# Performance work log

Hardware: AMD Instinct MI355X
Metric: run time of the kernel (lower is better)

## Reference

```python
import jax, jax.numpy as jnp
import numpy as np

DIM, H, HD = 1024, 16, 64
B, S = 2, 2048
LAMBDA_INIT = 0.8


def _mha(x, wq, bq, wk, bk, wv, bv, wo, bo):
    # x: [B,S,DIM]; wq/wk/wv: [DIM,H,HD]; wo: [H,HD,DIM]
    q = jnp.einsum('btd,dhk->bthk', x, wq) + bq
    k = jnp.einsum('bsd,dhk->bshk', x, wk) + bk
    v = jnp.einsum('bsd,dhk->bshk', x, wv) + bv
    scores = jnp.einsum('bthk,bshk->bhts', q, k) / jnp.sqrt(jnp.asarray(HD, x.dtype))
    attn = jax.nn.softmax(scores, axis=-1)
    out = jnp.einsum('bhts,bshk->bthk', attn, v)
    return jnp.einsum('bthk,hkd->btd', out, wo) + bo


def _get_lambda(lambda_param, layer_idx):
    layer_factor = jnp.clip(jnp.asarray(layer_idx, jnp.float32) * 0.3, 0.0, 5.0)
    offset = 0.6 * jnp.exp(-layer_factor)
    lam = jax.nn.sigmoid(lambda_param) * (1.0 - offset) + 0.2
    return jnp.clip(lam, 0.1, 0.9)


def setup_inputs() -> dict:
    key = jax.random.key(0)
    ks = jax.random.split(key, 10)
    sc_in = 1.0 / np.sqrt(DIM)   # fan-in-ish scale for projections
    sc_out = 1.0 / np.sqrt(H * HD)
    d = {
        'x': jax.random.normal(ks[0], (B, S, DIM), jnp.float32),
        'proj_w': jax.random.normal(ks[1], (DIM, DIM), jnp.float32) * sc_in,
        'proj_b': jnp.zeros((DIM,), jnp.float32),
        'lambda_param': jnp.full((1,), np.log(LAMBDA_INIT) - np.log(1.0 - LAMBDA_INIT), jnp.float32),
        'layer_idx': 0,
    }
    for i, kk in zip((1, 2), (ks[2:6], ks[6:10])):
        d[f'wq{i}'] = jax.random.normal(kk[0], (DIM, H, HD), jnp.float32) * sc_in
        d[f'wk{i}'] = jax.random.normal(kk[1], (DIM, H, HD), jnp.float32) * sc_in
        d[f'wv{i}'] = jax.random.normal(kk[2], (DIM, H, HD), jnp.float32) * sc_in
        d[f'wo{i}'] = jax.random.normal(kk[3], (H, HD, DIM), jnp.float32) * sc_out
        d[f'bq{i}'] = jnp.zeros((H, HD), jnp.float32)
        d[f'bk{i}'] = jnp.zeros((H, HD), jnp.float32)
        d[f'bv{i}'] = jnp.zeros((H, HD), jnp.float32)
        d[f'bo{i}'] = jnp.zeros((DIM,), jnp.float32)
    return d


def reference(x, wq1, bq1, wk1, bk1, wv1, bv1, wo1, bo1,
              wq2, bq2, wk2, bk2, wv2, bv2, wo2, bo2,
              proj_w, proj_b, lambda_param, layer_idx):
    out1 = _mha(x, wq1, bq1, wk1, bk1, wv1, bv1, wo1, bo1)
    out2 = _mha(x, wq2, bq2, wk2, bk2, wv2, bv2, wo2, bo2)
    lam = _get_lambda(lambda_param, layer_idx)  # shape (1,)
    y = (1.0 - lam) * out1 + lam * out2
    return jnp.einsum('btd,de->bte', y, proj_w) + proj_b
```

## Files before the change

### kernel.cpp

```cpp
#include <hip/hip_runtime.h>

#define DEVI __device__ __forceinline__

typedef unsigned short u16;
typedef unsigned int u32;
typedef __bf16 bf16x8 __attribute__((ext_vector_type(8)));
typedef float f32x4 __attribute__((ext_vector_type(4)));
typedef float f32x16 __attribute__((ext_vector_type(16)));
typedef int i32x2v __attribute__((ext_vector_type(2)));

#define SCALE_Q 0.1803368801f

typedef const __attribute__((address_space(1))) void cas1_void;
typedef __attribute__((address_space(3))) void as3_void;

DEVI void lds_dma16(const void* g, void* l) {
  __builtin_amdgcn_global_load_lds((cas1_void*)g, (as3_void*)l, 16, 0, 0);
}

DEVI u16 f2bf(float f) {
  union { float f; u32 u; } v; v.f = f;
  u32 r = v.u + 0x7FFFu + ((v.u >> 16) & 1u);
  return (u16)(r >> 16);
}

DEVI float bf2f(u16 v) {
  union { u32 u; float f; } x; x.u = (u32)v << 16; return x.f;
}

DEVI float exp2n(float x) {
#if __has_builtin(__builtin_amdgcn_exp2f)
  return __builtin_amdgcn_exp2f(x);
#else
  return __expf(x * 0.6931471805599453f);
#endif
}

DEVI u32 pk2(float lo, float hi2) {
  union { __bf16 h[2]; u32 u; } p;
  p.h[0] = (__bf16)lo; p.h[1] = (__bf16)hi2;
  return p.u;
}

DEVI void plswap2(u32 a, u32 b, u32& x, u32& y) {
#if __has_builtin(__builtin_amdgcn_permlane32_swap)
  i32x2v r = __builtin_amdgcn_permlane32_swap((int)a, (int)b, false, false);
  x = (u32)r[0]; y = (u32)r[1];
#else
  u32 ta = __shfl_xor(a, 32), tb = __shfl_xor(b, 32);
  const int hi_ = (int)((threadIdx.x & 63) >> 5);
  x = hi_ ? tb : a;
  y = hi_ ? b : ta;
#endif
}

DEVI float lambda_dev(const float* lamp, const int* lidx) {
  float lf = (float)(*lidx) * 0.3f;
  lf = fminf(fmaxf(lf, 0.0f), 5.0f);
  float offset = 0.6f * expf(-lf);
  float s = 1.0f / (1.0f + expf(-lamp[0]));
  float lam = s * (1.0f - offset) + 0.2f;
  return fminf(fmaxf(lam, 0.1f), 0.9f);
}

__global__ __launch_bounds__(256) void k_cvt(const float* __restrict__ x, u16* __restrict__ o) {
  int i = (blockIdx.x * 256 + threadIdx.x) * 8;
  float4 a = *(const float4*)(x + i);
  float4 b = *(const float4*)(x + i + 4);
  union { u16 s[8]; uint4 v; } r;
  r.s[0] = f2bf(a.x); r.s[1] = f2bf(a.y); r.s[2] = f2bf(a.z); r.s[3] = f2bf(a.w);
  r.s[4] = f2bf(b.x); r.s[5] = f2bf(b.y); r.s[6] = f2bf(b.z); r.s[7] = f2bf(b.w);
  *(uint4*)(o + i) = r.v;
}

struct TransArgs {
  const float* src[9];
  u16* dst[9];
  int smode[9];
  int tmode[9];
};

__global__ __launch_bounds__(256) void k_transpose(TransArgs ta, const float* lamp, const int* lidx) {
  __shared__ float tile[32][33];
  int z = blockIdx.z;
  int tx = threadIdx.x & 31, ty = threadIdx.x >> 5;
  int bx = blockIdx.x * 32, by = blockIdx.y * 32;
  const float* s = ta.src[z];
  float sc = 1.0f;
  int m = ta.smode[z];
  if (m == 1) sc = SCALE_Q;
  else if (m >= 2) {
    float lam = lambda_dev(lamp, lidx);
    sc = (m == 2) ? (1.0f - lam) : lam;
  }
  u16* d = ta.dst[z];
  if (ta.tmode[z]) {
#pragma unroll
    for (int i = 0; i < 4; ++i)
      tile[ty + i * 8][tx] = s[(size_t)(by + ty + i * 8) * 1024 + bx + tx];
    __syncthreads();
#pragma unroll
    for (int i = 0; i < 4; ++i) {
      int dr = bx + ty + i * 8;
      d[(size_t)dr * 1024 + by + tx] = f2bf(sc * tile[tx][ty + i * 8]);
    }
  } else {
#pragma unroll
    for (int i = 0; i < 4; ++i) {
      int r = by + ty + i * 8;
      d[(size_t)r * 1024 + bx + tx] = f2bf(sc * s[(size_t)r * 1024 + bx + tx]);
    }
  }
}

__global__ __launch_bounds__(256) void k_bias2(const u16* __restrict__ PWt, const float* __restrict__ bo1,
                                               const float* __restrict__ bo2, const float* __restrict__ pb,
                                               const float* lamp, const int* lidx, float* __restrict__ b2) {
  const float lam = lambda_dev(lamp, lidx);
  const int lane = threadIdx.x & 63;
  const int wv = blockIdx.x * 4 + (threadIdx.x >> 6);
#pragma unroll
  for (int i = 0; i < 4; ++i) {
    const int e = wv * 4 + i;
    const u16* row = PWt + (size_t)e * 1024 + lane * 16;
    float acc = 0.f;
#pragma unroll
    for (int j = 0; j < 16; ++j) {
      const int dd = lane * 16 + j;
      const float bm = (1.0f - lam) * bo1[dd] + lam * bo2[dd];
      acc += bf2f(row[j]) * bm;
    }
    acc += __shfl_xor(acc, 1);  acc += __shfl_xor(acc, 2);
    acc += __shfl_xor(acc, 4);  acc += __shfl_xor(acc, 8);
    acc += __shfl_xor(acc, 16); acc += __shfl_xor(acc, 32);
    if (lane == 0) b2[e] = acc + pb[e];
  }
}

struct GemmArgs {
  const u16* A;
  const u16* Bt;
  const float* bias0[6];
  float bscale[6];
  u16* dstu[6];
  u16* dst3;
  float* dstf;
  int K;
  int mode;
};

__global__ __launch_bounds__(256) void k_gemm(GemmArgs ga) {
  __shared__ __align__(16) u16 smem[32768];
  char* smc = (char*)smem;
  const int t = threadIdx.x;
  const int lane = t & 63;
  const int l15 = lane & 15, hi = lane >> 4;
  const int w = t >> 6, wm = w >> 1, wn = w & 1;
  int m0, n0, z;
  if (ga.mode == 0) {
    const int bid = blockIdx.x;
    const int xcd = bid & 7, local = bid >> 3;
    const int nb = xcd * 6 + (local % 6);
    m0 = (local / 6) * 128;
    n0 = nb * 128;
    z = n0 >> 10;
  } else {
    m0 = blockIdx.y * 128; n0 = blockIdx.x * 128; z = 0;
  }
  const u16* A = ga.A;
  const u16* Bt = ga.Bt;
  const int K = ga.K;

  const char* gA[4];
  const char* gB[4];
  u32 lof[4];
#pragma unroll
  for (int ii = 0; ii < 4; ++ii) {
    int fl = ii * 256 + t;
    int row = fl >> 3;
    int cb = ((fl & 7) * 16) ^ ((row & 7) << 4);
    gA[ii] = (const char*)(A + (size_t)(m0 + row) * K) + cb;
    gB[ii] = (const char*)(Bt + (size_t)(n0 + row) * K) + cb;
    lof[ii] = (u32)(ii * 256 + (t & ~63)) * 16;
  }

  u32 aoff[4], boff[4];
#pragma unroll
  for (int i = 0; i < 4; ++i) {
    int rA = wm * 64 + i * 16 + l15;
    aoff[i] = (u32)rA * 128 + (u32)((hi * 16) ^ ((rA & 7) << 4));
    int rB = wn * 64 + i * 16 + l15;
    boff[i] = 16384u + (u32)rB * 128 + (u32)((hi * 16) ^ ((rB & 7) << 4));
  }

  const f32x4 fz = {0.f, 0.f, 0.f, 0.f};
  f32x4 acc[4][4];
#pragma unroll
  for (int i = 0; i < 4; ++i)
#pragma unroll
    for (int j = 0; j < 4; ++j) acc[i][j] = fz;

  const int NT = K >> 6;
#pragma unroll
  for (int ii = 0; ii < 4; ++ii) {
    lds_dma16(gA[ii], smc + lof[ii]);
    lds_dma16(gB[ii], smc + 16384 + lof[ii]);
  }
  __syncthreads();
  int cur = 0;
  for (int kt = 0; kt < NT; ++kt) {
    if (kt + 1 < NT) {
      const u32 nb2 = (u32)(cur ^ 1) * 32768u;
      size_t soff = (size_t)(kt + 1) * 128;
#pragma unroll
      for (int ii = 0; ii < 4; ++ii) {
        lds_dma16(gA[ii] + soff, smc + nb2 + lof[ii]);
        lds_dma16(gB[ii] + soff, smc + nb2 + 16384 + lof[ii]);
      }
    }
    const u32 bb = (u32)cur * 32768u;
#pragma unroll
    for (int kh = 0; kh < 2; ++kh) {
      const u32 kx = (u32)kh << 6;
      bf16x8 af[4], bfr[4];
#pragma unroll
      for (int i = 0; i < 4; ++i) af[i] = *(const bf16x8*)(smc + bb + (aoff[i] ^ kx));
#pragma unroll
      for (int j = 0; j < 4; ++j) bfr[j] = *(const bf16x8*)(smc + bb + (boff[j] ^ kx));
#pragma unroll
      for (int i = 0; i < 4; ++i)
#pragma unroll
        for (int j = 0; j < 4; ++j)
          acc[i][j] = __builtin_amdgcn_mfma_f32_16x16x32_bf16(af[i], bfr[j], acc[i][j], 0, 0, 0);
    }
    __syncthreads();
    cur ^= 1;
  }

  const int mode = ga.mode;
  const float* b0 = ga.bias0[(mode == 0) ? z : 0];
  const float bsc = (mode == 0) ? ga.bscale[z] : 1.0f;
  const int kind = z % 3;
  u16* du = ga.dstu[z];

#pragma unroll
  for (int i = 0; i < 4; ++i) {
#pragma unroll
    for (int j = 0; j < 4; ++j) {
#pragma unroll
      for (int jj = 0; jj < 4; ++jj) {
        int m = m0 + wm * 64 + i * 16 + hi * 4 + jj;
        int n = n0 + wn * 64 + j * 16 + l15;
        float v = acc[i][j][jj];
        if (mode == 0) {
          int nz = n & 1023;
          v += b0[nz] * bsc;
          int b = m >> 11, s = m & 2047, h = nz >> 6, hd = nz & 63;
          size_t addr;
          if (kind == 0) {
            addr = ((size_t)(b * 16 + h) * 2048 + s) * 64 + hd;
          } else if (kind == 1) {
            int gf = ((s >> 5) * 8 + (hd >> 4) * 2 + ((hd >> 3) & 1)) * 32 + (s & 31);
            addr = ((size_t)(b * 16 + h) * 16384 + gf) * 8 + (hd & 7);
          } else {
            int gf = ((((s >> 6) * 4 + ((s >> 4) & 3)) * 2 + ((s >> 3) & 1)) * 2 + (hd >> 5)) * 32 + (hd & 31);
            addr = ((size_t)(b * 16 + h) * 16384 + gf) * 8 + (s & 7);
          }
          du[addr] = f2bf(v);
        } else if (mode == 3) {
          ga.dst3[(size_t)m * 2048 + n] = f2bf(v);
        } else {
          v += b0[n];
          ga.dstf[(size_t)m * 1024 + n] = v;
        }
      }
    }
  }
}

__global__ __launch_bounds__(256, 2) void k_attn3(const u16* __restrict__ Qg_, const u16* __restrict__ Kg_,
                                                  const u16* __restrict__ Vg_, u16* __restrict__ AO) {
  const int t = threadIdx.x, lane = t & 63, w = t >> 6;
  const int l31 = lane & 31, hi = lane >> 5;
  const int bid = blockIdx.x;
  const int xcd = bid & 7, slot = bid >> 3;
  const int qt = slot & 15;
  const int bhbr = xcd * 8 + (slot >> 4);
  const int br = bhbr >> 5, bh = bhbr & 31;
  const size_t base = ((size_t)br * 32 + bh) * 131072;
  const u16* Qg = Qg_ + base;
  const u16* Kt = Kg_ + base + (size_t)(hi * 256 + l31 * 8);
  const u16* Vt = Vg_ + base + (size_t)(hi * 512 + l31 * 8);
  const int q0 = qt * 128 + w * 32;

  bf16x8 qf[4];
  {
    const u16* qp = Qg + (size_t)(q0 + l31) * 64 + hi * 8;
#pragma unroll
    for (int ks = 0; ks < 4; ++ks) qf[ks] = *(const bf16x8*)(qp + ks * 16);
  }

  f32x16 accO[2];
#pragma unroll
  for (int b = 0; b < 2; ++b)
#pragma unroll
    for (int r = 0; r < 16; ++r) accO[b][r] = 0.f;
  float l_r = 0.f;

  bf16x8 kf[2][4], vf[2][4];
#pragma unroll
  for (int kvs = 0; kvs < 2; ++kvs)
#pragma unroll
    for (int ks = 0; ks < 4; ++ks)
      kf[kvs][ks] = *(const bf16x8*)(Kt + kvs * 2048 + ks * 512);
#pragma unroll
  for (int hs = 0; hs < 2; ++hs)
#pragma unroll
    for (int ks = 0; ks < 4; ++ks)
      vf[hs][ks] = *(const bf16x8*)(Vt + ks * 1024 + hs * 256);

  for (int kvt = 0; kvt < 32; ++kvt) {
    f32x16 st[2];
#pragma unroll
    for (int kvs = 0; kvs < 2; ++kvs)
#pragma unroll
      for (int r = 0; r < 16; ++r) st[kvs][r] = 0.f;
#pragma unroll
    for (int ks = 0; ks < 4; ++ks) {
      st[0] = __builtin_amdgcn_mfma_f32_32x32x16_bf16(kf[0][ks], qf[ks], st[0], 0, 0, 0);
      st[1] = __builtin_amdgcn_mfma_f32_32x32x16_bf16(kf[1][ks], qf[ks], st[1], 0, 0, 0);
    }
    if (kvt < 31) {
      const u16* kp = Kt + (size_t)(kvt + 1) * 4096;
#pragma unroll
      for (int kvs = 0; kvs < 2; ++kvs)
#pragma unroll
        for (int ks = 0; ks < 4; ++ks)
          kf[kvs][ks] = *(const bf16x8*)(kp + kvs * 2048 + ks * 512);
    }

    float sm0 = 0.f, sm1 = 0.f, sm2 = 0.f, sm3 = 0.f;
#pragma unroll
    for (int kvs = 0; kvs < 2; ++kvs)
#pragma unroll
      for (int r = 0; r < 16; r += 4) {
        float p0 = exp2n(st[kvs][r + 0]); st[kvs][r + 0] = p0; sm0 += p0;
        float p1 = exp2n(st[kvs][r + 1]); st[kvs][r + 1] = p1; sm1 += p1;
        float p2 = exp2n(st[kvs][r + 2]); st[kvs][r + 2] = p2; sm2 += p2;
        float p3 = exp2n(st[kvs][r + 3]); st[kvs][r + 3] = p3; sm3 += p3;
      }
    float sum = (sm0 + sm1) + (sm2 + sm3);
    sum += __shfl_xor(sum, 32);
    l_r += sum;

    bf16x8 pa[4];
#pragma unroll
    for (int kvs = 0; kvs < 2; ++kvs)
#pragma unroll
      for (int half = 0; half < 2; ++half) {
        const int rb = half * 8;
        u32 a0 = pk2(st[kvs][rb + 0], st[kvs][rb + 1]);
        u32 a1 = pk2(st[kvs][rb + 2], st[kvs][rb + 3]);
        u32 b0 = pk2(st[kvs][rb + 4], st[kvs][rb + 5]);
        u32 b1 = pk2(st[kvs][rb + 6], st[kvs][rb + 7]);
        u32 w0, w1, w2, w3;
        plswap2(a0, b0, w0, w2);
        plswap2(a1, b1, w1, w3);
        union { u32 u[4]; bf16x8 v; } pk;
        pk.u[0] = w0; pk.u[1] = w1; pk.u[2] = w2; pk.u[3] = w3;
        pa[kvs * 2 + half] = pk.v;
      }

#pragma unroll
    for (int ks = 0; ks < 4; ++ks) {
      accO[0] = __builtin_amdgcn_mfma_f32_32x32x16_bf16(pa[ks], vf[0][ks], accO[0], 0, 0, 0);
      accO[1] = __builtin_amdgcn_mfma_f32_32x32x16_bf16(pa[ks], vf[1][ks], accO[1], 0, 0, 0);
    }
    if (kvt < 31) {
      const u16* vp = Vt + (size_t)(kvt + 1) * 4096;
#pragma unroll
      for (int hs = 0; hs < 2; ++hs)
#pragma unroll
        for (int ks = 0; ks < 4; ++ks)
          vf[hs][ks] = *(const bf16x8*)(vp + ks * 1024 + hs * 256);
    }
  }

  const int b = bh >> 4, h = bh & 15;
  const float inv = 1.0f / l_r;
#pragma unroll
  for (int r = 0; r < 16; ++r) {
    const int qr = (r & 3) + 8 * (r >> 2) + 4 * hi;
    const float iv = __shfl(inv, qr);
    const size_t mrow = (size_t)(b * 2048 + q0 + qr);
#pragma unroll
    for (int hs = 0; hs < 2; ++hs) {
      const int col = br * 1024 + h * 64 + hs * 32 + l31;
      AO[mrow * 2048 + col] = f2bf(accO[hs][r] * iv);
    }
  }
}

extern "C" void kernel_launch(void* const* d_in, const int* in_sizes, int n_in,
                              void* d_out, int out_size, void* d_ws, size_t ws_size,
                              hipStream_t stream) {
  (void)in_sizes; (void)n_in; (void)out_size; (void)ws_size;
  const float* x      = (const float*)d_in[0];
  const float* proj_w = (const float*)d_in[1];
  const float* proj_b = (const float*)d_in[2];
  const float* lamp   = (const float*)d_in[3];
  const int*   lidx   = (const int*)d_in[4];
  const float* wq1 = (const float*)d_in[5];
  const float* wk1 = (const float*)d_in[6];
  const float* wv1 = (const float*)d_in[7];
  const float* wo1 = (const float*)d_in[8];
  const float* bq1 = (const float*)d_in[9];
  const float* bk1 = (const float*)d_in[10];
  const float* bv1 = (const float*)d_in[11];
  const float* bo1 = (const float*)d_in[12];
  const float* wq2 = (const float*)d_in[13];
  const float* wk2 = (const float*)d_in[14];
  const float* wv2 = (const float*)d_in[15];
  const float* wo2 = (const float*)d_in[16];
  const float* bq2 = (const float*)d_in[17];
  const float* bk2 = (const float*)d_in[18];
  const float* bv2 = (const float*)d_in[19];
  const float* bo2 = (const float*)d_in[20];

  char* ws = (char*)d_ws;
  const size_t MB = 1024 * 1024;
  u16* xb   = (u16*)(ws);
  u16* Wt   = (u16*)(ws + 8 * MB);
  u16* WOt2 = (u16*)(ws + 20 * MB);
  u16* PWt  = (u16*)(ws + 24 * MB);
  u16* Qb   = (u16*)(ws + 26 * MB);
  u16* Kb   = (u16*)(ws + 42 * MB);
  u16* Vb   = (u16*)(ws + 58 * MB);
  u16* Bt2  = (u16*)(ws + 74 * MB);
  float* b2 = (float*)(ws + 78 * MB);
  u16* AOb  = (u16*)(ws);

  k_cvt<<<2048, 256, 0, stream>>>(x, xb);

  TransArgs ta;
  const float* srcs[9] = {wq1, wk1, wv1, wq2, wk2, wv2, wo1, wo2, proj_w};
  u16* dsts[9] = {Wt, Wt + 1048576, Wt + 2097152, Wt + 3145728, Wt + 4194304, Wt + 5242880,
                  WOt2, WOt2 + 1048576, PWt};
  int smode[9] = {1, 0, 0, 1, 0, 0, 2, 3, 0};
  int tmode[9] = {1, 1, 1, 1, 1, 1, 0, 0, 1};
  for (int i = 0; i < 9; ++i) {
    ta.src[i] = srcs[i]; ta.dst[i] = dsts[i];
    ta.smode[i] = smode[i]; ta.tmode[i] = tmode[i];
  }
  k_transpose<<<dim3(32, 32, 9), 256, 0, stream>>>(ta, lamp, lidx);

  GemmArgs gw = {};
  gw.A = PWt; gw.Bt = WOt2; gw.dst3 = Bt2; gw.K = 1024; gw.mode = 3;
  k_gemm<<<dim3(16, 8), 256, 0, stream>>>(gw);

  k_bias2<<<64, 256, 0, stream>>>(PWt, bo1, bo2, proj_b, lamp, lidx, b2);

  GemmArgs g0 = {};
  g0.A = xb; g0.Bt = Wt; g0.K = 1024; g0.mode = 0;
  const float* qkvb[6] = {bq1, bk1, bv1, bq2, bk2, bv2};
  const size_t BRS = 4194304;
  u16* qkvd[6] = {Qb, Kb, Vb, Qb + BRS, Kb + BRS, Vb + BRS};
  float bsc[6] = {SCALE_Q, 1.f, 1.f, SCALE_Q, 1.f, 1.f};
  for (int i = 0; i < 6; ++i) {
    g0.bias0[i] = qkvb[i];
    g0.bscale[i] = bsc[i];
    g0.dstu[i] = qkvd[i];
  }
  k_gemm<<<dim3(1536), 256, 0, stream>>>(g0);

  k_attn3<<<1024, 256, 0, stream>>>(Qb, Kb, Vb, AOb);

  GemmArgs g2 = {};
  g2.A = AOb; g2.Bt = Bt2; g2.K = 2048; g2.mode = 2;
  g2.bias0[0] = b2;
  g2.dstf = (float*)d_out;
  k_gemm<<<dim3(8, 32), 256, 0, stream>>>(g2);
}
```

Baseline: 271.5 us.

## Single-buffer GEMM LDS for higher occupancy and fold weight GEMM into QKV launch

The GEMM kernel drops its double-buffered LDS pipeline for a single 32KB buffer and raises launch bounds to allow four blocks per CU, relying on occupancy rather than in-block prefetch to hide load latency. The separate weight-combination GEMM (proj_w times wo) is merged into the QKV projection launch as 128 extra blocks, which removes one kernel launch. Because the prefetch is gone, each k-step now waits on its own global loads, and that stall has to be covered by the other resident blocks.

Result: faster. 252.3 us (-7.1%).

```diff
diff --git a/kernel.cpp b/kernel.cpp
--- a/kernel.cpp
+++ b/kernel.cpp
@@ -140,6 +140,8 @@
 struct GemmArgs {
   const u16* A;
   const u16* Bt;
+  const u16* A2;
+  const u16* Bt2p;
   const float* bias0[6];
   float bscale[6];
   u16* dstu[6];
@@ -149,27 +151,37 @@
   int mode;
 };
 
-__global__ __launch_bounds__(256) void k_gemm(GemmArgs ga) {
-  __shared__ __align__(16) u16 smem[32768];
+__global__ __launch_bounds__(256, 4) void k_gemm(GemmArgs ga) {
+  __shared__ __align__(16) u16 smem[16384];
   char* smc = (char*)smem;
   const int t = threadIdx.x;
   const int lane = t & 63;
   const int l15 = lane & 15, hi = lane >> 4;
   const int w = t >> 6, wm = w >> 1, wn = w & 1;
-  int m0, n0, z;
-  if (ga.mode == 0) {
+  int m0, n0, z, K, mode = ga.mode;
+  const u16* A;
+  const u16* Bt;
+  if (mode == 0) {
     const int bid = blockIdx.x;
-    const int xcd = bid & 7, local = bid >> 3;
-    const int nb = xcd * 6 + (local % 6);
-    m0 = (local / 6) * 128;
-    n0 = nb * 128;
-    z = n0 >> 10;
+    if (bid >= 1536) {
+      mode = 3;
+      const int lb = bid - 1536;
+      m0 = (lb >> 4) * 128;
+      n0 = (lb & 15) * 128;
+      z = 0;
+      A = ga.A2; Bt = ga.Bt2p; K = 1024;
+    } else {
+      const int xcd = bid & 7, local = bid >> 3;
+      const int nb = xcd * 6 + (local % 6);
+      m0 = (local / 6) * 128;
+      n0 = nb * 128;
+      z = n0 >> 10;
+      A = ga.A; Bt = ga.Bt; K = ga.K;
+    }
   } else {
     m0 = blockIdx.y * 128; n0 = blockIdx.x * 128; z = 0;
-  }
-  const u16* A = ga.A;
-  const u16* Bt = ga.Bt;
-  const int K = ga.K;
+    A = ga.A; Bt = ga.Bt; K = ga.K;
+  }
 
   const char* gA[4];
   const char* gB[4];
@@ -201,32 +213,22 @@
     for (int j = 0; j < 4; ++j) acc[i][j] = fz;
 
   const int NT = K >> 6;
-#pragma unroll
-  for (int ii = 0; ii < 4; ++ii) {
-    lds_dma16(gA[ii], smc + lof[ii]);
-    lds_dma16(gB[ii], smc + 16384 + lof[ii]);
-  }
-  __syncthreads();
-  int cur = 0;
   for (int kt = 0; kt < NT; ++kt) {
-    if (kt + 1 < NT) {
-      const u32 nb2 = (u32)(cur ^ 1) * 32768u;
-      size_t soff = (size_t)(kt + 1) * 128;
-#pragma unroll
-      for (int ii = 0; ii < 4; ++ii) {
-        lds_dma16(gA[ii] + soff, smc + nb2 + lof[ii]);
-        lds_dma16(gB[ii] + soff, smc + nb2 + 16384 + lof[ii]);
-      }
-    }
-    const u32 bb = (u32)cur * 32768u;
+    const size_t soff = (size_t)kt * 128;
+#pragma unroll
+    for (int ii = 0; ii < 4; ++ii) {
+      lds_dma16(gA[ii] + soff, smc + lof[ii]);
+      lds_dma16(gB[ii] + soff, smc + 16384 + lof[ii]);
+    }
+    __syncthreads();
 #pragma unroll
     for (int kh = 0; kh < 2; ++kh) {
       const u32 kx = (u32)kh << 6;
       bf16x8 af[4], bfr[4];
 #pragma unroll
-      for (int i = 0; i < 4; ++i) af[i] = *(const bf16x8*)(smc + bb + (aoff[i] ^ kx));
-#pragma unroll
-      for (int j = 0; j < 4; ++j) bfr[j] = *(const bf16x8*)(smc + bb + (boff[j] ^ kx));
+      for (int i = 0; i < 4; ++i) af[i] = *(const bf16x8*)(smc + (aoff[i] ^ kx));
+#pragma unroll
+      for (int j = 0; j < 4; ++j) bfr[j] = *(const bf16x8*)(smc + (boff[j] ^ kx));
 #pragma unroll
       for (int i = 0; i < 4; ++i)
 #pragma unroll
@@ -234,10 +236,8 @@
           acc[i][j] = __builtin_amdgcn_mfma_f32_16x16x32_bf16(af[i], bfr[j], acc[i][j], 0, 0, 0);
     }
     __syncthreads();
-    cur ^= 1;
-  }
-
-  const int mode = ga.mode;
+  }
+
   const float* b0 = ga.bias0[(mode == 0) ? z : 0];
   const float bsc = (mode == 0) ? ga.bscale[z] : 1.0f;
   const int kind = z % 3;
@@ -454,14 +454,11 @@
   }
   k_transpose<<<dim3(32, 32, 9), 256, 0, stream>>>(ta, lamp, lidx);
 
-  GemmArgs gw = {};
-  gw.A = PWt; gw.Bt = WOt2; gw.dst3 = Bt2; gw.K = 1024; gw.mode = 3;
-  k_gemm<<<dim3(16, 8), 256, 0, stream>>>(gw);
-
   k_bias2<<<64, 256, 0, stream>>>(PWt, bo1, bo2, proj_b, lamp, lidx, b2);
 
   GemmArgs g0 = {};
   g0.A = xb; g0.Bt = Wt; g0.K = 1024; g0.mode = 0;
+  g0.A2 = PWt; g0.Bt2p = WOt2; g0.dst3 = Bt2;
   const float* qkvb[6] = {bq1, bk1, bv1, bq2, bk2, bv2};
   const size_t BRS = 4194304;
   u16* qkvd[6] = {Qb, Kb, Vb, Qb + BRS, Kb + BRS, Vb + BRS};
@@ -471,7 +468,7 @@
     g0.bscale[i] = bsc[i];
     g0.dstu[i] = qkvd[i];
   }
-  k_gemm<<<dim3(1536), 256, 0, stream>>>(g0);
+  k_gemm<<<dim3(1664), 256, 0, stream>>>(g0);
 
   k_attn3<<<1024, 256, 0, stream>>>(Qb, Kb, Vb, AOb);
 
```
